# Performance work log

Hardware: AMD Instinct MI355X
Metric: run time of the kernel (lower is better)

The kernel has to match this reference:

```python
import jax, jax.numpy as jnp
import numpy as np

N_DRUG = 50000
N_PROT = 50000
E = 1000000
H = 128

def setup_inputs() -> dict:
    key = jax.random.key(0)
    k1, k2, k3, k4, k5 = jax.random.split(key, 5)
    z_drug = jax.random.normal(k1, (N_DRUG, H), dtype=jnp.float32)
    z_protein = jax.random.normal(k2, (N_PROT, H), dtype=jnp.float32)
    edge_label_index = jax.random.randint(k3, (2, E), 0, N_DRUG, dtype=jnp.int64)
    # Linear params (Kaiming-ish scale)
    W1 = jax.random.normal(k4, (H, 2 * H), dtype=jnp.float32) / np.sqrt(2 * H)
    b1 = jnp.zeros((H,), dtype=jnp.float32)
    W2 = jax.random.normal(k5, (1, H), dtype=jnp.float32) / np.sqrt(H)
    b2 = jnp.zeros((1,), dtype=jnp.float32)
    return {"z_drug": z_drug, "z_protein": z_protein,
            "edge_label_index": edge_label_index,
            "W1": W1, "b1": b1, "W2": W2, "b2": b2}

def reference(z_drug, z_protein, edge_label_index, W1, b1, W2, b2):
    row, col = edge_label_index[0], edge_label_index[1]
    # gather node embeddings along edges, concat -> [E, 2H]
    z = jnp.concatenate([z_drug[row], z_protein[col]], axis=-1)
    h = jax.nn.relu(jnp.einsum('eh,oh->eo', z, W1) + b1)  # [E, H]
    out = jnp.einsum('eh,oh->eo', h, W2) + b2             # [E, 1]
    return out.reshape(-1)
```

## Files before the change

kernel.cpp:

```cpp
#include <hip/hip_runtime.h>


typedef __attribute__((ext_vector_type(8))) short bhalf8;
typedef __attribute__((ext_vector_type(4))) float f32x4;

__device__ __forceinline__ unsigned bfr(float f) {
    unsigned u = __builtin_bit_cast(unsigned, f);
    return (u + 0x7fffu + ((u >> 16) & 1u)) >> 16;
}
__device__ __forceinline__ unsigned pk2(float a, float b) {
    return bfr(a) | (bfr(b) << 16);
}
__device__ __forceinline__ float db(unsigned w, int b) {
    return (float)(int)(signed char)((w >> (b * 8)) & 0xffu);
}

#define SH_STRIDE 132

__global__ __launch_bounds__(512) void hprepq_kernel(
    const float* __restrict__ zd, const float* __restrict__ zp,
    const float* __restrict__ W1, const float* __restrict__ b1,
    signed char* __restrict__ Hd, signed char* __restrict__ Hp,
    float* __restrict__ scD, float* __restrict__ scP,
    int Nd, int Np, int nbd)
{
    __shared__ __align__(16) char smem[64 * SH_STRIDE * 4];
    short* sZ = (short*)smem;
    float* sH = (float*)smem;

    const bool isP = (int)blockIdx.x >= nbd;
    const float* z = isP ? zp : zd;
    signed char* H = isP ? Hp : Hd;
    float* sc = isP ? scP : scD;
    const int N    = isP ? Np : Nd;
    const int koff = isP ? 128 : 0;
    const int blk  = isP ? blockIdx.x - nbd : blockIdx.x;

    const int tid  = threadIdx.x;
    const int wave = tid >> 6;
    const int lane = tid & 63;
    const int l15  = lane & 15;
    const int lhi  = lane >> 4;
    const int ocol = wave * 16 + l15;

    bhalf8 bfrag[4];
    #pragma unroll
    for (int ks = 0; ks < 4; ++ks) {
        const float4* src = (const float4*)(W1 + ocol * 256 + koff + ks * 32 + lhi * 8);
        float4 p = src[0], q = src[1];
        bhalf8 f;
        f[0] = (short)bfr(p.x); f[1] = (short)bfr(p.y);
        f[2] = (short)bfr(p.z); f[3] = (short)bfr(p.w);
        f[4] = (short)bfr(q.x); f[5] = (short)bfr(q.y);
        f[6] = (short)bfr(q.z); f[7] = (short)bfr(q.w);
        bfrag[ks] = f;
    }
    const float bias = isP ? 0.0f : b1[ocol];
    const int r0 = blk * 64;

    {
        const int rl = tid >> 3;
        const int grow = min(r0 + rl, N - 1);
        const float4* zr = (const float4*)(z + (size_t)grow * 128);
        #pragma unroll
        for (int q = 0; q < 4; ++q) {
            const int s = (tid & 7) + q * 8;
            float4 v = zr[s];
            uint2 w; w.x = pk2(v.x, v.y); w.y = pk2(v.z, v.w);
            int byte = (rl * 256 + s * 8) ^ ((rl & 7) << 4);
            *(uint2*)((char*)sZ + byte) = w;
        }
    }
    __syncthreads();

    f32x4 acc[4] = {{0.f,0.f,0.f,0.f},{0.f,0.f,0.f,0.f},
                    {0.f,0.f,0.f,0.f},{0.f,0.f,0.f,0.f}};
    #pragma unroll
    for (int ks = 0; ks < 4; ++ks) {
        #pragma unroll
        for (int rt = 0; rt < 4; ++rt) {
            const int row = rt * 16 + l15;
            int byte = (row * 256 + ks * 64 + lhi * 16) ^ ((row & 7) << 4);
            bhalf8 af = *(const bhalf8*)((const char*)sZ + byte);
            acc[rt] = __builtin_amdgcn_mfma_f32_16x16x32_bf16(af, bfrag[ks], acc[rt], 0, 0, 0);
        }
    }
    __syncthreads();

    #pragma unroll
    for (int rt = 0; rt < 4; ++rt) {
        #pragma unroll
        for (int i = 0; i < 4; ++i) {
            const int row = rt * 16 + lhi * 4 + i;
            sH[row * SH_STRIDE + ocol] = acc[rt][i] + bias;
        }
    }
    __syncthreads();

    {
        const int qrow = tid >> 3;
        const int k    = tid & 7;
        float4 v4[4];
        float mx = 0.0f;
        #pragma unroll
        for (int j = 0; j < 4; ++j) {
            v4[j] = *(const float4*)(sH + qrow * SH_STRIDE + k * 16 + j * 4);
            mx = fmaxf(mx, fmaxf(fmaxf(fabsf(v4[j].x), fabsf(v4[j].y)),
                                 fmaxf(fabsf(v4[j].z), fabsf(v4[j].w))));
        }
        mx = fmaxf(mx, __shfl_xor(mx, 1, 64));
        mx = fmaxf(mx, __shfl_xor(mx, 2, 64));
        mx = fmaxf(mx, __shfl_xor(mx, 4, 64));
        const float inv = 127.0f / fmaxf(mx, 1e-20f);
        uint4 o;
        unsigned ob[4];
        #pragma unroll
        for (int j = 0; j < 4; ++j) {
            int a0 = __float2int_rn(v4[j].x * inv);
            int a1 = __float2int_rn(v4[j].y * inv);
            int a2 = __float2int_rn(v4[j].z * inv);
            int a3 = __float2int_rn(v4[j].w * inv);
            ob[j] = (unsigned)(a0 & 0xff) | ((unsigned)(a1 & 0xff) << 8) |
                    ((unsigned)(a2 & 0xff) << 16) | ((unsigned)(a3 & 0xff) << 24);
        }
        o.x = ob[0]; o.y = ob[1]; o.z = ob[2]; o.w = ob[3];
        const int grow = r0 + qrow;
        if (grow < N) {
            *(uint4*)(H + (size_t)grow * 128 + k * 16) = o;
            if (k == 0) sc[grow] = mx * (1.0f / 127.0f);
        }
    }
}

__global__ __launch_bounds__(256, 4) void edgeq_kernel(
    const signed char* __restrict__ Hd, const signed char* __restrict__ Hp,
    const float* __restrict__ scD, const float* __restrict__ scP,
    const int* __restrict__ eli, const float* __restrict__ W2,
    const float* __restrict__ b2, float* __restrict__ out, int E)
{
    const int sub = threadIdx.x & 15;
    const int grp = threadIdx.x >> 4;
    float4 w2a = ((const float4*)W2)[sub * 2];
    float4 w2b = ((const float4*)W2)[sub * 2 + 1];
    const float b2v = b2[0];

    const int EPB = 16 * 8;
    const int step = gridDim.x * EPB;
    int base = blockIdx.x * EPB;
    if (base >= E) return;

    int row[8], col[8];
    #pragma unroll
    for (int u = 0; u < 8; ++u) {
        const int e = base + grp * 8 + u;
        row[u] = (e < E) ? eli[e] : 0;
        col[u] = (e < E) ? eli[E + e] : 0;
    }

    for (; base < E; base += step) {
        uint2 qd[8], qp[8];
        float sd[8], sp[8];
        #pragma unroll
        for (int u = 0; u < 8; ++u) {
            qd[u] = *(const uint2*)(Hd + (size_t)row[u] * 128 + sub * 8);
            qp[u] = *(const uint2*)(Hp + (size_t)col[u] * 128 + sub * 8);
            sd[u] = scD[row[u]];
            sp[u] = scP[col[u]];
        }
        const int nb = base + step;
        if (nb < E) {
            #pragma unroll
            for (int u = 0; u < 8; ++u) {
                const int e = nb + grp * 8 + u;
                row[u] = (e < E) ? eli[e] : 0;
                col[u] = (e < E) ? eli[E + e] : 0;
            }
        }
        #pragma unroll
        for (int u = 0; u < 8; ++u) {
            float s = 0.f;
            const unsigned dx = qd[u].x, dy = qd[u].y;
            const unsigned px = qp[u].x, py = qp[u].y;
            s = fmaf(fmaxf(db(dx,0) * sd[u] + db(px,0) * sp[u], 0.f), w2a.x, s);
            s = fmaf(fmaxf(db(dx,1) * sd[u] + db(px,1) * sp[u], 0.f), w2a.y, s);
            s = fmaf(fmaxf(db(dx,2) * sd[u] + db(px,2) * sp[u], 0.f), w2a.z, s);
            s = fmaf(fmaxf(db(dx,3) * sd[u] + db(px,3) * sp[u], 0.f), w2a.w, s);
            s = fmaf(fmaxf(db(dy,0) * sd[u] + db(py,0) * sp[u], 0.f), w2b.x, s);
            s = fmaf(fmaxf(db(dy,1) * sd[u] + db(py,1) * sp[u], 0.f), w2b.y, s);
            s = fmaf(fmaxf(db(dy,2) * sd[u] + db(py,2) * sp[u], 0.f), w2b.z, s);
            s = fmaf(fmaxf(db(dy,3) * sd[u] + db(py,3) * sp[u], 0.f), w2b.w, s);
            s += __shfl_xor(s, 1, 64);
            s += __shfl_xor(s, 2, 64);
            s += __shfl_xor(s, 4, 64);
            s += __shfl_xor(s, 8, 64);
            const int e = base + grp * 8 + u;
            if (sub == 0 && e < E) out[e] = s + b2v;
        }
    }
}

#define TE 64
__global__ __launch_bounds__(512, 4) void ec_fallback(
    const float* __restrict__ zd, const float* __restrict__ zp,
    const int* __restrict__ eli, const float* __restrict__ W1,
    const float* __restrict__ b1, const float* __restrict__ W2,
    const float* __restrict__ b2, float* __restrict__ out,
    int E, int nTiles)
{
    __shared__ __align__(16) short sZ[TE * 256];
    __shared__ float sPart[8][TE];
    const int tid  = threadIdx.x;
    const int wave = tid >> 6;
    const int lane = tid & 63;
    const int l15  = lane & 15;
    const int lhi  = lane >> 4;
    const int ocol = wave * 16 + l15;
    bhalf8 bfrag[8];
    #pragma unroll
    for (int ks = 0; ks < 8; ++ks) {
        const float4* src = (const float4*)(W1 + ocol * 256 + ks * 32 + lhi * 8);
        float4 p = src[0], q = src[1];
        bhalf8 f;
        f[0] = (short)bfr(p.x); f[1] = (short)bfr(p.y);
        f[2] = (short)bfr(p.z); f[3] = (short)bfr(p.w);
        f[4] = (short)bfr(q.x); f[5] = (short)bfr(q.y);
        f[6] = (short)bfr(q.z); f[7] = (short)bfr(q.w);
        bfrag[ks] = f;
    }
    const float b1v = b1[ocol];
    const float w2v = W2[ocol];
    const float b2v = b2[0];
    const int slot = tid >> 5;
    const int lane32 = tid & 31;
    for (int tile = blockIdx.x; tile < nTiles; tile += gridDim.x) {
        const int base = tile * TE;
        __syncthreads();
        #pragma unroll
        for (int r = 0; r < 4; ++r) {
            const int e  = slot * 4 + r;
            const int eg = base + e;
            int drow = 0, pcol = 0;
            if (eg < E) { drow = eli[eg]; pcol = eli[E + eg]; }
            float4 v = ((const float4*)(zd + (size_t)drow * 128))[lane32];
            float4 u = ((const float4*)(zp + (size_t)pcol * 128))[lane32];
            int byte0 = (e * 512 + lane32 * 8) ^ ((e & 7) << 4);
            uint2 pv; pv.x = pk2(v.x, v.y); pv.y = pk2(v.z, v.w);
            *(uint2*)((char*)sZ + byte0) = pv;
            int byte1 = (e * 512 + 256 + lane32 * 8) ^ ((e & 7) << 4);
            uint2 pu; pu.x = pk2(u.x, u.y); pu.y = pk2(u.z, u.w);
            *(uint2*)((char*)sZ + byte1) = pu;
        }
        __syncthreads();
        f32x4 acc[4] = {{0.f,0.f,0.f,0.f},{0.f,0.f,0.f,0.f},
                        {0.f,0.f,0.f,0.f},{0.f,0.f,0.f,0.f}};
        #pragma unroll
        for (int ks = 0; ks < 8; ++ks) {
            const int kb = (ks * 32 + lhi * 8) * 2;
            #pragma unroll
            for (int rt = 0; rt < 4; ++rt) {
                const int row = rt * 16 + l15;
                int byte = (row * 512 + kb) ^ ((row & 7) << 4);
                bhalf8 af = *(const bhalf8*)((const char*)sZ + byte);
                acc[rt] = __builtin_amdgcn_mfma_f32_16x16x32_bf16(af, bfrag[ks], acc[rt], 0, 0, 0);
            }
        }
        #pragma unroll
        for (int rt = 0; rt < 4; ++rt) {
            #pragma unroll
            for (int i = 0; i < 4; ++i) {
                float v = acc[rt][i] + b1v;
                v = fmaxf(v, 0.0f) * w2v;
                v += __shfl_xor(v, 1, 64);
                v += __shfl_xor(v, 2, 64);
                v += __shfl_xor(v, 4, 64);
                v += __shfl_xor(v, 8, 64);
                if (l15 == 0) sPart[wave][rt * 16 + lhi * 4 + i] = v;
            }
        }
        __syncthreads();
        if (tid < TE) {
            const int eg = base + tid;
            if (eg < E) {
                float s = b2v;
                #pragma unroll
                for (int w = 0; w < 8; ++w) s += sPart[w][tid];
                out[eg] = s;
            }
        }
    }
}

extern "C" void kernel_launch(void* const* d_in, const int* in_sizes, int n_in,
                              void* d_out, int out_size, void* d_ws, size_t ws_size,
                              hipStream_t stream) {
    const float* zd = (const float*)d_in[0];
    const float* zp = (const float*)d_in[1];
    const int*   eli = (const int*)d_in[2];
    const float* W1 = (const float*)d_in[3];
    const float* b1 = (const float*)d_in[4];
    const float* W2 = (const float*)d_in[5];
    const float* b2 = (const float*)d_in[6];
    float* out = (float*)d_out;

    const int E  = in_sizes[2] / 2;
    const int nd = in_sizes[0];
    const int np = in_sizes[1];
    const int Nd = nd / 128, Np = np / 128;
    const int nbd = (Nd + 63) / 64, nbp = (Np + 63) / 64;

    const size_t offHp = (size_t)Nd * 128;
    const size_t offSd = (offHp + (size_t)Np * 128 + 15) & ~(size_t)15;
    const size_t offSp = offSd + (size_t)Nd * sizeof(float);
    const size_t need  = offSp + (size_t)Np * sizeof(float);

    if (ws_size >= need) {
        signed char* Hd = (signed char*)d_ws;
        signed char* Hp = Hd + offHp;
        float* scD = (float*)((char*)d_ws + offSd);
        float* scP = (float*)((char*)d_ws + offSp);
        hipLaunchKernelGGL(hprepq_kernel, dim3(nbd + nbp), dim3(512), 0, stream,
                           zd, zp, W1, b1, Hd, Hp, scD, scP, Nd, Np, nbd);
        hipLaunchKernelGGL(edgeq_kernel, dim3(4096), dim3(256), 0, stream,
                           Hd, Hp, scD, scP, eli, W2, b2, out, E);
    } else {
        const int nTiles = (E + TE - 1) / TE;
        hipLaunchKernelGGL(ec_fallback, dim3(2048), dim3(512), 0, stream,
                           zd, zp, eli, W1, b1, W2, b2, out, E, nTiles);
    }
}
```

Measured before the change: 65.44 us.

## Widen edge gather to 16-byte loads and factor out drug scale

Each edge is now handled by 8 lanes, each loading 16 bytes per row with uint4 loads instead of 16 lanes loading 8 bytes. This shortens the shuffle reduction by one step. The per-element dequantization is rewritten as relu(d + r*p) with r = sp/sd, and sd is applied once at the output since relu is positively homogeneous. That saves one multiply per element. The clamp of sd to 1e-25 and the approximate reciprocal add small rounding differences and a risk for zero-scale rows.

Result: faster. 58.51 us (-10.6%).

```diff
diff --git a/kernel.cpp b/kernel.cpp
--- a/kernel.cpp
+++ b/kernel.cpp
@@ -138,63 +138,66 @@
     const int* __restrict__ eli, const float* __restrict__ W2,
     const float* __restrict__ b2, float* __restrict__ out, int E)
 {
-    const int sub = threadIdx.x & 15;
-    const int grp = threadIdx.x >> 4;
-    float4 w2a = ((const float4*)W2)[sub * 2];
-    float4 w2b = ((const float4*)W2)[sub * 2 + 1];
+    const int sub = threadIdx.x & 7;
+    const int grp = threadIdx.x >> 3;
+    float4 w2[4];
+    #pragma unroll
+    for (int j = 0; j < 4; ++j) w2[j] = ((const float4*)W2)[sub * 4 + j];
     const float b2v = b2[0];
 
-    const int EPB = 16 * 8;
+    const int EPB = 32 * 4;
     const int step = gridDim.x * EPB;
     int base = blockIdx.x * EPB;
     if (base >= E) return;
 
-    int row[8], col[8];
-    #pragma unroll
-    for (int u = 0; u < 8; ++u) {
-        const int e = base + grp * 8 + u;
+    int row[4], col[4];
+    #pragma unroll
+    for (int u = 0; u < 4; ++u) {
+        const int e = base + grp * 4 + u;
         row[u] = (e < E) ? eli[e] : 0;
         col[u] = (e < E) ? eli[E + e] : 0;
     }
 
     for (; base < E; base += step) {
-        uint2 qd[8], qp[8];
-        float sd[8], sp[8];
-        #pragma unroll
-        for (int u = 0; u < 8; ++u) {
-            qd[u] = *(const uint2*)(Hd + (size_t)row[u] * 128 + sub * 8);
-            qp[u] = *(const uint2*)(Hp + (size_t)col[u] * 128 + sub * 8);
-            sd[u] = scD[row[u]];
-            sp[u] = scP[col[u]];
+        uint4 qd[4], qp[4];
+        float sdc[4], r[4];
+        #pragma unroll
+        for (int u = 0; u < 4; ++u) {
+            qd[u] = *(const uint4*)(Hd + (size_t)row[u] * 128 + sub * 16);
+            qp[u] = *(const uint4*)(Hp + (size_t)col[u] * 128 + sub * 16);
+            const float sd = scD[row[u]];
+            const float sp = scP[col[u]];
+            sdc[u] = fmaxf(sd, 1e-25f);
+            r[u]   = sp * __builtin_amdgcn_rcpf(sdc[u]);
         }
         const int nb = base + step;
         if (nb < E) {
             #pragma unroll
-            for (int u = 0; u < 8; ++u) {
-                const int e = nb + grp * 8 + u;
+            for (int u = 0; u < 4; ++u) {
+                const int e = nb + grp * 4 + u;
                 row[u] = (e < E) ? eli[e] : 0;
                 col[u] = (e < E) ? eli[E + e] : 0;
             }
         }
         #pragma unroll
-        for (int u = 0; u < 8; ++u) {
+        for (int u = 0; u < 4; ++u) {
+            const float ru = r[u];
             float s = 0.f;
-            const unsigned dx = qd[u].x, dy = qd[u].y;
-            const unsigned px = qp[u].x, py = qp[u].y;
-            s = fmaf(fmaxf(db(dx,0) * sd[u] + db(px,0) * sp[u], 0.f), w2a.x, s);
-            s = fmaf(fmaxf(db(dx,1) * sd[u] + db(px,1) * sp[u], 0.f), w2a.y, s);
-            s = fmaf(fmaxf(db(dx,2) * sd[u] + db(px,2) * sp[u], 0.f), w2a.z, s);
-            s = fmaf(fmaxf(db(dx,3) * sd[u] + db(px,3) * sp[u], 0.f), w2a.w, s);
-            s = fmaf(fmaxf(db(dy,0) * sd[u] + db(py,0) * sp[u], 0.f), w2b.x, s);
-            s = fmaf(fmaxf(db(dy,1) * sd[u] + db(py,1) * sp[u], 0.f), w2b.y, s);
-            s = fmaf(fmaxf(db(dy,2) * sd[u] + db(py,2) * sp[u], 0.f), w2b.z, s);
-            s = fmaf(fmaxf(db(dy,3) * sd[u] + db(py,3) * sp[u], 0.f), w2b.w, s);
+            const unsigned dws[4] = {qd[u].x, qd[u].y, qd[u].z, qd[u].w};
+            const unsigned pws[4] = {qp[u].x, qp[u].y, qp[u].z, qp[u].w};
+            #pragma unroll
+            for (int j = 0; j < 4; ++j) {
+                const unsigned d = dws[j], p = pws[j];
+                s = fmaf(fmaxf(fmaf(ru, db(p,0), db(d,0)), 0.f), w2[j].x, s);
+                s = fmaf(fmaxf(fmaf(ru, db(p,1), db(d,1)), 0.f), w2[j].y, s);
+                s = fmaf(fmaxf(fmaf(ru, db(p,2), db(d,2)), 0.f), w2[j].z, s);
+                s = fmaf(fmaxf(fmaf(ru, db(p,3), db(d,3)), 0.f), w2[j].w, s);
+            }
             s += __shfl_xor(s, 1, 64);
             s += __shfl_xor(s, 2, 64);
             s += __shfl_xor(s, 4, 64);
-            s += __shfl_xor(s, 8, 64);
-            const int e = base + grp * 8 + u;
-            if (sub == 0 && e < E) out[e] = s + b2v;
+            const int e = base + grp * 4 + u;
+            if (sub == 0 && e < E) out[e] = fmaf(s, sdc[u], b2v);
         }
     }
 }
```
